# Kernel optimization log

Measured on AMD Instinct MI355X. Metric: run time of the kernel, lower is better.

The kernel has to match this reference:

```python
import jax, jax.numpy as jnp
import numpy as np

TEMP = 10.0
BPE = 4
BER = 0.01
K = 2 ** BPE  # number of centers


def setup_inputs() -> dict:
    key = jax.random.key(0)
    k1, k2 = jax.random.split(key)
    x = jax.random.normal(k1, (32, 256, 32, 32), dtype=jnp.float32)
    center = jax.random.normal(k2, (K,), dtype=jnp.float32)
    return {"x": x, "center": center}


def reference(x, center):
    # Q_type == 'Soft' path of quantizer_channel.forward
    # residuals to every center: [B, C, H, W, K]
    d = x[..., None] - center
    # nearest-center index (hard assignment)
    W_index = jnp.argmin(jnp.abs(d), axis=-1)  # int32 [B,C,H,W]
    # soft assignment and soft quantized value
    smx = jax.nn.softmax(-TEMP * (d * d), axis=-1)
    W_soft = jnp.einsum('bchwk,k->bchw', smx, center)
    # bitmap rows are the binary expansion of the index, MSB first;
    # map[W_index][..., j] == (W_index >> (BPE-1-j)) & 1
    shifts = jnp.arange(BPE - 1, -1, -1, dtype=jnp.int32)  # [BPE]
    bits = (W_index[..., None] >> shifts) & 1  # [B,C,H,W,BPE]
    # bernoulli bit-flip channel noise; (bit + noise) % 2 == XOR
    noise = jax.random.bernoulli(jax.random.key(42), BER, bits.shape).astype(bits.dtype)
    noisy_bits = bits ^ noise
    # index = sum_i 2^i * bits[..., BPE-1-i]  ==  dot with 2^shifts
    idx_noisy = jnp.sum(noisy_bits * (2 ** shifts), axis=-1)
    W_noisy = center[idx_noisy]
    # soft value with stop-gradient channel bias (straight-through noise)
    return W_soft + jax.lax.stop_gradient(W_noisy - W_soft)
```

## Files before the change

### kernel.cpp

```cpp
#include <hip/hip_runtime.h>
#include <stdint.h>


#define KS1 42u
#define KS2 0x1BD11BF0u
#define BERN_LT 42950144u

__device__ __forceinline__ uint32_t fkey(float f) {
  uint32_t u = __float_as_uint(f);
  return (u & 0x80000000u) ? ~u : (u | 0x80000000u);
}
__device__ __forceinline__ float finv(uint32_t k) {
  uint32_t u = (k & 0x80000000u) ? (k & 0x7fffffffu) : ~k;
  return __uint_as_float(u);
}

__global__ void quantizer_setup_kernel(const float* __restrict__ center,
                                       float* __restrict__ ws) {
  const int t = threadIdx.x;
  __shared__ float sval[16];
  __shared__ int   sidx[16];
  if (t < 16) {
    const float ct = center[t];
    int rank = 0;
    for (int j = 0; j < 16; ++j) {
      const float cj = center[j];
      rank += (cj < ct || (cj == ct && j < t)) ? 1 : 0;
    }
    sval[rank] = ct;
    sidx[rank] = t;
  }
  __syncthreads();
  if (t < 15) {
    const float sL = sval[t], sR = sval[t + 1];
    const bool tieLeft = sidx[t] < sidx[t + 1];
    uint32_t lo = fkey(sL), hi = fkey(sR);
    while (hi - lo > 1u) {
      const uint32_t mid = lo + ((hi - lo) >> 1);
      const float xm = finv(mid);
      const float dL = fabsf(xm - sL);
      const float dR = fabsf(xm - sR);
      const bool left = (dL < dR) || (dL == dR && tieLeft);
      if (left) lo = mid; else hi = mid;
    }
    ws[t] = finv(lo);
  }
  __syncthreads();
  if (t < 16) {
    ((uint32_t*)ws)[16 + t] = (uint32_t)sidx[t];
    if (t == 15) ((uint32_t*)ws)[15] = 0u;
  }
}

__device__ __forceinline__ uint32_t rotl(uint32_t x, int r) {
  return __builtin_amdgcn_alignbit(x, x, (32 - r) & 31);
}
#define TF_ROUND4(r)                                            \
  { _Pragma("unroll") for (int j = 0; j < 4; ++j) {             \
      y0[j] += y1[j];                                           \
      y1[j] = rotl(y1[j], (r)) ^ y0[j];                         \
  } }
#define TF_INJ4(a, b)                                           \
  { _Pragma("unroll") for (int j = 0; j < 4; ++j) {             \
      y0[j] += (a); y1[j] += (b);                               \
  } }
#define TF_BODY                                                 \
  TF_ROUND4(13) TF_ROUND4(15) TF_ROUND4(26) TF_ROUND4(6)       \
  TF_INJ4(KS1, KS2 + 1u)                                        \
  TF_ROUND4(17) TF_ROUND4(29) TF_ROUND4(16) TF_ROUND4(24)      \
  TF_INJ4(KS2, 0u + 2u)                                         \
  TF_ROUND4(13) TF_ROUND4(15) TF_ROUND4(26) TF_ROUND4(6)       \
  TF_INJ4(0u, KS1 + 3u)                                         \
  TF_ROUND4(17) TF_ROUND4(29) TF_ROUND4(16) TF_ROUND4(24)      \
  TF_INJ4(KS1, KS2 + 4u)                                        \
  TF_ROUND4(13) TF_ROUND4(15) TF_ROUND4(26) TF_ROUND4(6)       \
  TF_INJ4(KS2, 0u + 5u)

__global__ __launch_bounds__(1024) void quantizer_channel_kernel(
    const float* __restrict__ x, const float* __restrict__ center,
    const float* __restrict__ ws, float* __restrict__ out,
    int n4, int nthreads)
{
  const int t = blockIdx.x * blockDim.x + threadIdx.x;

  const int lane   = threadIdx.x & 63;
  const int base_b = (lane & 48) << 2;

  const int ctab = __float_as_int(center[lane & 15]);
  const int stab = (int)((const uint32_t*)ws)[16 + (lane & 15)];

  const float4* wsf = (const float4*)ws;
  const float4 ta = wsf[0], tb = wsf[1], tc = wsf[2], td = wsf[3];
  const float T0 = ta.x, T1 = ta.y, T2  = ta.z, T3  = ta.w;
  const float T4 = tb.x, T5 = tb.y, T6  = tb.z, T7  = tb.w;
  const float T8 = tc.x, T9 = tc.y, T10 = tc.z, T11 = tc.w;
  const float T12 = td.x, T13 = td.y, T14 = td.z;

#pragma unroll
  for (int pass = 0; pass < 2; ++pass) {
    const int i = t + pass * nthreads;
    if (i >= n4) break;

    const float4 xv = reinterpret_cast<const float4*>(x)[i];
    const float xe[4] = {xv.x, xv.y, xv.z, xv.w};
    float oe[4];
    const uint32_t cb = (uint32_t)i * 16u + KS1;

#pragma unroll
    for (int e = 0; e < 4; ++e) {
      uint32_t y0[4], y1[4];
      const uint32_t c0 = cb + 4u * (uint32_t)e;
#pragma unroll
      for (int j = 0; j < 4; ++j) { y0[j] = 0u; y1[j] = c0 + (uint32_t)j; }
      TF_BODY

      uint32_t f = 0u;
      f = f + f + (((y0[0] ^ y1[0]) < BERN_LT) ? 1u : 0u);
      f = f + f + (((y0[1] ^ y1[1]) < BERN_LT) ? 1u : 0u);
      f = f + f + (((y0[2] ^ y1[2]) < BERN_LT) ? 1u : 0u);
      f = f + f + (((y0[3] ^ y1[3]) < BERN_LT) ? 1u : 0u);

      const float v = xe[e];
      const bool b3_ = v > T7;
      const float s2 = b3_ ? T11 : T3;
      const bool b2_ = v > s2;
      const float s1 = b3_ ? (b2_ ? T13 : T9) : (b2_ ? T5 : T1);
      const bool b1_ = v > s1;
      const float u0 = b1_ ? T2  : T0;
      const float u1 = b1_ ? T6  : T4;
      const float u2 = b1_ ? T10 : T8;
      const float u3 = b1_ ? T14 : T12;
      const float s0 = b3_ ? (b2_ ? u3 : u2) : (b2_ ? u1 : u0);
      const bool b0_ = v > s0;
      const uint32_t cell = (b3_ ? 8u : 0u) | (b2_ ? 4u : 0u) |
                            (b1_ ? 2u : 0u) | (b0_ ? 1u : 0u);

      const int best = __builtin_amdgcn_ds_bpermute(base_b + (int)(cell << 2), stab);
      const int fin_addr = base_b + (int)((((uint32_t)best) ^ f) << 2);
      oe[e] = __int_as_float(__builtin_amdgcn_ds_bpermute(fin_addr, ctab));
    }

    float4 o4;
    o4.x = oe[0]; o4.y = oe[1]; o4.z = oe[2]; o4.w = oe[3];
    reinterpret_cast<float4*>(out)[i] = o4;
  }
}

extern "C" void kernel_launch(void* const* d_in, const int* in_sizes, int n_in,
                              void* d_out, int out_size, void* d_ws, size_t ws_size,
                              hipStream_t stream)
{
  const float* x      = (const float*)d_in[0];
  const float* center = (const float*)d_in[1];
  float* out          = (float*)d_out;
  float* ws           = (float*)d_ws;

  hipLaunchKernelGGL(quantizer_setup_kernel, dim3(1), dim3(64), 0, stream,
                     center, ws);

  const int N  = in_sizes[0];
  const int n4 = N / 4;
  const int block = 1024;
  const int nthreads = (n4 + 1) / 2;
  const int grid  = (nthreads + block - 1) / block;

  hipLaunchKernelGGL(quantizer_channel_kernel, dim3(grid), dim3(block), 0, stream,
                     x, center, ws, out, n4, grid * block);
}
```

Baseline: 73.79 us.

## Use grid-stride loop with next-load prefetch and trim first Threefry round

Replaces the fixed two-pass-per-thread launch with a grid-stride loop over 2048 blocks of 256 threads. Each iteration issues the load for the next float4 before computing the current one, so memory latency overlaps the Threefry hashing. The first Threefry round is simplified because y0 starts at zero, which saves one add per lane. The trade-off is fewer resident threads to hide latency, plus a dependence on the loop structure to get the overlap.

```diff
diff --git a/kernel.cpp b/kernel.cpp
--- a/kernel.cpp
+++ b/kernel.cpp
@@ -64,8 +64,12 @@
   { _Pragma("unroll") for (int j = 0; j < 4; ++j) {             \
       y0[j] += (a); y1[j] += (b);                               \
   } }
-#define TF_BODY                                                 \
-  TF_ROUND4(13) TF_ROUND4(15) TF_ROUND4(26) TF_ROUND4(6)       \
+#define TF_BODY_FROM_CTR                                        \
+  { _Pragma("unroll") for (int j = 0; j < 4; ++j) {             \
+      y0[j] = y1[j];                                            \
+      y1[j] = rotl(y1[j], 13) ^ y0[j];                          \
+  } }                                                           \
+  TF_ROUND4(15) TF_ROUND4(26) TF_ROUND4(6)                      \
   TF_INJ4(KS1, KS2 + 1u)                                        \
   TF_ROUND4(17) TF_ROUND4(29) TF_ROUND4(16) TF_ROUND4(24)      \
   TF_INJ4(KS2, 0u + 2u)                                         \
@@ -76,12 +80,12 @@
   TF_ROUND4(13) TF_ROUND4(15) TF_ROUND4(26) TF_ROUND4(6)       \
   TF_INJ4(KS2, 0u + 5u)
 
-__global__ __launch_bounds__(1024) void quantizer_channel_kernel(
+__global__ __launch_bounds__(256) void quantizer_channel_kernel(
     const float* __restrict__ x, const float* __restrict__ center,
     const float* __restrict__ ws, float* __restrict__ out,
-    int n4, int nthreads)
+    int n4, int stride)
 {
-  const int t = blockIdx.x * blockDim.x + threadIdx.x;
+  const int t0 = blockIdx.x * blockDim.x + threadIdx.x;
 
   const int lane   = threadIdx.x & 63;
   const int base_b = (lane & 48) << 2;
@@ -96,13 +100,18 @@
   const float T8 = tc.x, T9 = tc.y, T10 = tc.z, T11 = tc.w;
   const float T12 = td.x, T13 = td.y, T14 = td.z;
 
-#pragma unroll
-  for (int pass = 0; pass < 2; ++pass) {
-    const int i = t + pass * nthreads;
-    if (i >= n4) break;
+  const float4* __restrict__ x4  = reinterpret_cast<const float4*>(x);
+  float4* __restrict__       out4 = reinterpret_cast<float4*>(out);
 
-    const float4 xv = reinterpret_cast<const float4*>(x)[i];
-    const float xe[4] = {xv.x, xv.y, xv.z, xv.w};
+  if (t0 >= n4) return;
+  float4 xv = x4[t0];
+
+  for (int i = t0; i < n4; i += stride) {
+    const float4 cur = xv;
+    const int inext = i + stride;
+    if (inext < n4) xv = x4[inext];
+
+    const float xe[4] = {cur.x, cur.y, cur.z, cur.w};
     float oe[4];
     const uint32_t cb = (uint32_t)i * 16u + KS1;
 
@@ -111,8 +120,8 @@
       uint32_t y0[4], y1[4];
       const uint32_t c0 = cb + 4u * (uint32_t)e;
 #pragma unroll
-      for (int j = 0; j < 4; ++j) { y0[j] = 0u; y1[j] = c0 + (uint32_t)j; }
-      TF_BODY
+      for (int j = 0; j < 4; ++j) { y1[j] = c0 + (uint32_t)j; }
+      TF_BODY_FROM_CTR
 
       uint32_t f = 0u;
       f = f + f + (((y0[0] ^ y1[0]) < BERN_LT) ? 1u : 0u);
@@ -142,7 +151,7 @@
 
     float4 o4;
     o4.x = oe[0]; o4.y = oe[1]; o4.z = oe[2]; o4.w = oe[3];
-    reinterpret_cast<float4*>(out)[i] = o4;
+    out4[i] = o4;
   }
 }
 
@@ -160,9 +169,10 @@
 
   const int N  = in_sizes[0];
   const int n4 = N / 4;
-  const int block = 1024;
-  const int nthreads = (n4 + 1) / 2;
-  const int grid  = (nthreads + block - 1) / block;
+  const int block = 256;
+  int grid = 2048;
+  const int maxg = (n4 + block - 1) / block;
+  if (grid > maxg) grid = maxg;
 
   hipLaunchKernelGGL(quantizer_channel_kernel, dim3(grid), dim3(block), 0, stream,
                      x, center, ws, out, n4, grid * block);
```

Result: slower. 75.64 us (+2.5%).
